# Kernel tuning notes

Hardware: AMD Instinct MI355X
Metric: run time of the kernel (lower is better)

## Reference

```python
import jax, jax.numpy as jnp
import numpy as np


def _chamfer(src, tgt):
    # src: [B, N, 3], tgt: [B, M, 3]
    x2 = jnp.sum(src * src, axis=-1)              # [B, N]
    y2 = jnp.sum(tgt * tgt, axis=-1)              # [B, M]
    xy = jnp.einsum('bnd,bmd->bnm', src, tgt)     # [B, N, M]
    d2 = x2[:, :, None] + y2[:, None, :] - 2.0 * xy
    d2 = jnp.maximum(d2, 0.0)                     # guard tiny negatives
    cham_x = jnp.min(d2, axis=2)                  # [B, N] min over tgt
    cham_y = jnp.min(d2, axis=1)                  # [B, M] min over src
    # point_reduction='mean', batch_reduction='sum'
    loss = jnp.sum(jnp.mean(cham_x, axis=1)) + jnp.sum(jnp.mean(cham_y, axis=1))
    return loss


def setup_inputs() -> dict:
    key = jax.random.key(0)
    k1, k2 = jax.random.split(key)
    src = jax.random.normal(k1, (16, 4096, 3), dtype=jnp.float32)
    tgt = jax.random.normal(k2, (16, 4096, 3), dtype=jnp.float32)
    return {"src": src, "tgt": tgt}


def reference(src, tgt):
    wgeo = 1.0
    return wgeo * _chamfer(src, tgt)
```

## Files before the change

### kernel.cpp

```cpp
#include <hip/hip_runtime.h>
#include <hip/hip_bf16.h>


#define BATCH  16
#define NPTS   4096
#define NPER   (BATCH * NPTS)
#define CHUNKC 512
#define NCHUNKS (NPTS / CHUNKC)

typedef __attribute__((ext_vector_type(8)))  short short8;
typedef __attribute__((ext_vector_type(16))) float float16;

union U4S8 { uint4 u; short8 s; };

__device__ inline unsigned int bfb(float v) {
    __hip_bfloat16 h = __float2bfloat16(v);
    unsigned short u; __builtin_memcpy(&u, &h, 2);
    return (unsigned int)u;
}
__device__ inline float bff(float v) { return __bfloat162float(__float2bfloat16(v)); }

#define ONEB 0x3F80u

__global__ __launch_bounds__(256) void aug_kernel(
    const float* __restrict__ src, const float* __restrict__ tgt,
    uint4* __restrict__ layAlo, uint4* __restrict__ layAhi,
    uint4* __restrict__ layBlo, uint4* __restrict__ layBhi)
{
    int i = blockIdx.x * 256 + threadIdx.x;
    int role = i >> 16;
    int p = i & (NPER - 1);
    const float* base = role ? tgt : src;
    float x = base[3 * p + 0];
    float y = base[3 * p + 1];
    float z = base[3 * p + 2];

    float xhf = bff(x), yhf = bff(y), zhf = bff(z);
    float xlf = x - xhf, ylf = y - yhf, zlf = z - zhf;
    float f = fmaf(x, x, fmaf(y, y, z * z));
    float fhf = bff(f), flf = f - fhf;

    unsigned xh = bfb(xhf), yh = bfb(yhf), zh = bfb(zhf);
    unsigned xl = bfb(xlf), yl = bfb(ylf), zl = bfb(zlf);
    unsigned fh = bfb(fhf), fl = bfb(flf);

    uint4 aw0 = make_uint4(xh | (yh << 16), zh | (xh << 16),
                           yh | (zh << 16), xl | (yl << 16));
    uint4 aw1 = make_uint4(zl | (fh << 16), fl | (ONEB << 16), ONEB, 0u);
    unsigned a = bfb(-2.0f * xhf), b = bfb(-2.0f * yhf), c = bfb(-2.0f * zhf);
    unsigned d = bfb(-2.0f * xlf), e = bfb(-2.0f * ylf), g = bfb(-2.0f * zlf);
    uint4 bw0 = make_uint4(a | (b << 16), c | (d << 16),
                           e | (g << 16), a | (b << 16));
    uint4 bw1 = make_uint4(c | (ONEB << 16), ONEB | (fh << 16), fl, 0u);

    layAlo[i] = aw0; layAhi[i] = aw1;
    layBlo[i] = bw0; layBhi[i] = bw1;
}

__global__ __launch_bounds__(256, 4) void chamfer_mfma_kernel(
    const uint4* __restrict__ layAlo, const uint4* __restrict__ layAhi,
    const uint4* __restrict__ layBlo, const uint4* __restrict__ layBhi,
    float* __restrict__ out)
{
    __shared__ uint4 sbuf[2][2][CHUNKC];
    __shared__ float wsum[4];

    int blk = blockIdx.x;
    const int strip = blk & 31; blk >>= 5;
    const int b     = blk & 15; blk >>= 4;
    const int dir   = blk;

    const int lane = threadIdx.x & 63;
    const int w    = threadIdx.x >> 6;
    const int half = lane >> 5;
    const int l5   = lane & 31;

    const size_t Aoff = (size_t)dir * NPER + (size_t)b * NPTS;
    const size_t Boff = (size_t)(1 - dir) * NPER + (size_t)b * NPTS;

    U4S8 at; at.u = (half ? layAhi : layAlo)[Aoff + strip * 128 + w * 32 + l5];
    const short8 afr = at.s;

    const uint4* Blo = layBlo + Boff;
    const uint4* Bhi = layBhi + Boff;

    auto stage = [&](int c, int bi) {
#pragma unroll
        for (int j = 0; j < 4; j++) {
            int li = w * 256 + j * 64;
            int hf = li >> 9;
            int pt = li & (CHUNKC - 1);
            const uint4* gsrc = (hf ? Bhi : Blo) + c * CHUNKC + pt + lane;
            __builtin_amdgcn_global_load_lds(
                (const __attribute__((address_space(1))) unsigned int*)gsrc,
                (__attribute__((address_space(3))) unsigned int*)&sbuf[bi][hf][pt],
                16, 0, 0);
        }
    };

    const float16 z16 = {0.f,0.f,0.f,0.f,0.f,0.f,0.f,0.f,
                         0.f,0.f,0.f,0.f,0.f,0.f,0.f,0.f};
    float rm[16];
#pragma unroll
    for (int r = 0; r < 16; r++) rm[r] = 1e30f;

    stage(0, 0);
    for (int c = 0; c < NCHUNKS; c++) {
        __syncthreads();
        if (c + 1 < NCHUNKS) stage(c + 1, (c + 1) & 1);
        const int bi = c & 1;
#pragma unroll 2
        for (int j2 = 0; j2 < CHUNKC / 64; j2++) {
            U4S8 t0, t1;
            t0.u = sbuf[bi][half][j2 * 64 + l5];
            t1.u = sbuf[bi][half][j2 * 64 + 32 + l5];
            float16 a0 = __builtin_amdgcn_mfma_f32_32x32x16_bf16(afr, t0.s, z16, 0, 0, 0);
            float16 a1 = __builtin_amdgcn_mfma_f32_32x32x16_bf16(afr, t1.s, z16, 0, 0, 0);
#pragma unroll
            for (int r = 0; r < 16; r++)
                rm[r] = fminf(fminf(a0[r], a1[r]), rm[r]);
        }
    }

#pragma unroll
    for (int mask = 1; mask <= 16; mask <<= 1)
#pragma unroll
        for (int r = 0; r < 16; r++)
            rm[r] = fminf(rm[r], __shfl_xor(rm[r], mask, 64));

    float s = 0.0f;
#pragma unroll
    for (int r = 0; r < 16; r++) s += fmaxf(rm[r], 0.0f);
    s += __shfl_xor(s, 32, 64);

    if (lane == 0) wsum[w] = s;
    __syncthreads();
    if (threadIdx.x == 0)
        atomicAdd(out, (wsum[0] + wsum[1] + wsum[2] + wsum[3]) * (1.0f / (float)NPTS));
}

extern "C" void kernel_launch(void* const* d_in, const int* in_sizes, int n_in,
                              void* d_out, int out_size, void* d_ws, size_t ws_size,
                              hipStream_t stream)
{
    const float* src = (const float*)d_in[0];
    const float* tgt = (const float*)d_in[1];
    float* out = (float*)d_out;

    uint4* layAlo = (uint4*)d_ws;
    uint4* layAhi = layAlo + 2 * NPER;
    uint4* layBlo = layAhi + 2 * NPER;
    uint4* layBhi = layBlo + 2 * NPER;

    hipMemsetAsync(out, 0, sizeof(float), stream);
    aug_kernel<<<2 * NPER / 256, 256, 0, stream>>>(src, tgt,
                                                   layAlo, layAhi, layBlo, layBhi);
    chamfer_mfma_kernel<<<2 * BATCH * 32, 256, 0, stream>>>(layAlo, layAhi,
                                                            layBlo, layBhi, out);
}
```

Before: 88.18 us.

## Fuse bf16 split-layout prep into chamfer MFMA kernel and double rows per wave

Removes the separate augmentation kernel and its workspace round trip. The main kernel now reads raw xyz and builds the bf16 hi/lo augmented operands in registers, for its A rows and for each B chunk as it is written to LDS. Each wave now handles two 32-row A fragments, so every LDS B fragment feeds twice as many MFMAs, and the grid shrinks to 16 strips per batch and direction. The cost is redundant B conversion in every block, plain synchronous stores instead of async global-to-LDS loads, and more registers, with launch bounds lowered to 2 blocks per CU.

```diff
diff --git a/kernel.cpp b/kernel.cpp
--- a/kernel.cpp
+++ b/kernel.cpp
@@ -2,11 +2,11 @@
 #include <hip/hip_bf16.h>
 
 
-#define BATCH  16
-#define NPTS   4096
-#define NPER   (BATCH * NPTS)
-#define CHUNKC 512
+#define BATCH   16
+#define NPTS    4096
+#define CHUNKC  512
 #define NCHUNKS (NPTS / CHUNKC)
+#define NSTRIPS 16
 
 typedef __attribute__((ext_vector_type(8)))  short short8;
 typedef __attribute__((ext_vector_type(16))) float float16;
@@ -22,52 +22,41 @@
 
 #define ONEB 0x3F80u
 
-__global__ __launch_bounds__(256) void aug_kernel(
-    const float* __restrict__ src, const float* __restrict__ tgt,
-    uint4* __restrict__ layAlo, uint4* __restrict__ layAhi,
-    uint4* __restrict__ layBlo, uint4* __restrict__ layBhi)
-{
-    int i = blockIdx.x * 256 + threadIdx.x;
-    int role = i >> 16;
-    int p = i & (NPER - 1);
-    const float* base = role ? tgt : src;
-    float x = base[3 * p + 0];
-    float y = base[3 * p + 1];
-    float z = base[3 * p + 2];
-
+__device__ inline void buildA(float x, float y, float z, uint4& w0, uint4& w1) {
     float xhf = bff(x), yhf = bff(y), zhf = bff(z);
-    float xlf = x - xhf, ylf = y - yhf, zlf = z - zhf;
     float f = fmaf(x, x, fmaf(y, y, z * z));
-    float fhf = bff(f), flf = f - fhf;
-
+    float fhf = bff(f);
     unsigned xh = bfb(xhf), yh = bfb(yhf), zh = bfb(zhf);
-    unsigned xl = bfb(xlf), yl = bfb(ylf), zl = bfb(zlf);
-    unsigned fh = bfb(fhf), fl = bfb(flf);
-
-    uint4 aw0 = make_uint4(xh | (yh << 16), zh | (xh << 16),
-                           yh | (zh << 16), xl | (yl << 16));
-    uint4 aw1 = make_uint4(zl | (fh << 16), fl | (ONEB << 16), ONEB, 0u);
-    unsigned a = bfb(-2.0f * xhf), b = bfb(-2.0f * yhf), c = bfb(-2.0f * zhf);
-    unsigned d = bfb(-2.0f * xlf), e = bfb(-2.0f * ylf), g = bfb(-2.0f * zlf);
-    uint4 bw0 = make_uint4(a | (b << 16), c | (d << 16),
-                           e | (g << 16), a | (b << 16));
-    uint4 bw1 = make_uint4(c | (ONEB << 16), ONEB | (fh << 16), fl, 0u);
-
-    layAlo[i] = aw0; layAhi[i] = aw1;
-    layBlo[i] = bw0; layBhi[i] = bw1;
+    unsigned xl = bfb(x - xhf), yl = bfb(y - yhf), zl = bfb(z - zhf);
+    unsigned fh = bfb(fhf), fl = bfb(f - fhf);
+    w0 = make_uint4(xh | (yh << 16), zh | (xh << 16),
+                    yh | (zh << 16), xl | (yl << 16));
+    w1 = make_uint4(zl | (fh << 16), fl | (ONEB << 16), ONEB, 0u);
 }
 
-__global__ __launch_bounds__(256, 4) void chamfer_mfma_kernel(
-    const uint4* __restrict__ layAlo, const uint4* __restrict__ layAhi,
-    const uint4* __restrict__ layBlo, const uint4* __restrict__ layBhi,
+__device__ inline void buildB(float x, float y, float z, uint4& w0, uint4& w1) {
+    float xhf = bff(x), yhf = bff(y), zhf = bff(z);
+    float f = fmaf(x, x, fmaf(y, y, z * z));
+    float fhf = bff(f);
+    unsigned a = bfb(-2.0f * xhf), b = bfb(-2.0f * yhf), c = bfb(-2.0f * zhf);
+    unsigned d = bfb(-2.0f * (x - xhf)), e = bfb(-2.0f * (y - yhf)),
+             g = bfb(-2.0f * (z - zhf));
+    unsigned fh = bfb(fhf), fl = bfb(f - fhf);
+    w0 = make_uint4(a | (b << 16), c | (d << 16),
+                    e | (g << 16), a | (b << 16));
+    w1 = make_uint4(c | (ONEB << 16), ONEB | (fh << 16), fl, 0u);
+}
+
+__global__ __launch_bounds__(256, 2) void chamfer_fused_kernel(
+    const float* __restrict__ src, const float* __restrict__ tgt,
     float* __restrict__ out)
 {
     __shared__ uint4 sbuf[2][2][CHUNKC];
     __shared__ float wsum[4];
 
     int blk = blockIdx.x;
-    const int strip = blk & 31; blk >>= 5;
-    const int b     = blk & 15; blk >>= 4;
+    const int strip = blk & (NSTRIPS - 1); blk >>= 4;
+    const int b     = blk & 15;            blk >>= 4;
     const int dir   = blk;
 
     const int lane = threadIdx.x & 63;
@@ -75,62 +64,74 @@
     const int half = lane >> 5;
     const int l5   = lane & 31;
 
-    const size_t Aoff = (size_t)dir * NPER + (size_t)b * NPTS;
-    const size_t Boff = (size_t)(1 - dir) * NPER + (size_t)b * NPTS;
+    const float* Araw = (dir ? tgt : src) + (size_t)b * NPTS * 3;
+    const float* Braw = (dir ? src : tgt) + (size_t)b * NPTS * 3;
 
-    U4S8 at; at.u = (half ? layAhi : layAlo)[Aoff + strip * 128 + w * 32 + l5];
-    const short8 afr = at.s;
+    short8 afr[2];
+#pragma unroll
+    for (int g = 0; g < 2; g++) {
+        int row = strip * 256 + g * 128 + w * 32 + l5;
+        uint4 w0, w1;
+        buildA(Araw[3 * row], Araw[3 * row + 1], Araw[3 * row + 2], w0, w1);
+        U4S8 t; t.u = half ? w1 : w0;
+        afr[g] = t.s;
+    }
 
-    const uint4* Blo = layBlo + Boff;
-    const uint4* Bhi = layBhi + Boff;
-
-    auto stage = [&](int c, int bi) {
+    auto convert = [&](int c, int bi) {
 #pragma unroll
-        for (int j = 0; j < 4; j++) {
-            int li = w * 256 + j * 64;
-            int hf = li >> 9;
-            int pt = li & (CHUNKC - 1);
-            const uint4* gsrc = (hf ? Bhi : Blo) + c * CHUNKC + pt + lane;
-            __builtin_amdgcn_global_load_lds(
-                (const __attribute__((address_space(1))) unsigned int*)gsrc,
-                (__attribute__((address_space(3))) unsigned int*)&sbuf[bi][hf][pt],
-                16, 0, 0);
+        for (int k = 0; k < 2; k++) {
+            int lp = (int)threadIdx.x + k * 256;
+            int p  = c * CHUNKC + lp;
+            uint4 w0, w1;
+            buildB(Braw[3 * p], Braw[3 * p + 1], Braw[3 * p + 2], w0, w1);
+            sbuf[bi][0][lp] = w0;
+            sbuf[bi][1][lp] = w1;
         }
     };
 
     const float16 z16 = {0.f,0.f,0.f,0.f,0.f,0.f,0.f,0.f,
                          0.f,0.f,0.f,0.f,0.f,0.f,0.f,0.f};
-    float rm[16];
+    float rm[2][16];
 #pragma unroll
-    for (int r = 0; r < 16; r++) rm[r] = 1e30f;
+    for (int g = 0; g < 2; g++)
+#pragma unroll
+        for (int r = 0; r < 16; r++) rm[g][r] = 1e30f;
 
-    stage(0, 0);
+    convert(0, 0);
     for (int c = 0; c < NCHUNKS; c++) {
         __syncthreads();
-        if (c + 1 < NCHUNKS) stage(c + 1, (c + 1) & 1);
+        if (c + 1 < NCHUNKS) convert(c + 1, (c + 1) & 1);
         const int bi = c & 1;
 #pragma unroll 2
         for (int j2 = 0; j2 < CHUNKC / 64; j2++) {
             U4S8 t0, t1;
             t0.u = sbuf[bi][half][j2 * 64 + l5];
             t1.u = sbuf[bi][half][j2 * 64 + 32 + l5];
-            float16 a0 = __builtin_amdgcn_mfma_f32_32x32x16_bf16(afr, t0.s, z16, 0, 0, 0);
-            float16 a1 = __builtin_amdgcn_mfma_f32_32x32x16_bf16(afr, t1.s, z16, 0, 0, 0);
+            float16 a00 = __builtin_amdgcn_mfma_f32_32x32x16_bf16(afr[0], t0.s, z16, 0, 0, 0);
+            float16 a01 = __builtin_amdgcn_mfma_f32_32x32x16_bf16(afr[0], t1.s, z16, 0, 0, 0);
+            float16 a10 = __builtin_amdgcn_mfma_f32_32x32x16_bf16(afr[1], t0.s, z16, 0, 0, 0);
+            float16 a11 = __builtin_amdgcn_mfma_f32_32x32x16_bf16(afr[1], t1.s, z16, 0, 0, 0);
 #pragma unroll
-            for (int r = 0; r < 16; r++)
-                rm[r] = fminf(fminf(a0[r], a1[r]), rm[r]);
+            for (int r = 0; r < 16; r++) {
+                rm[0][r] = fminf(fminf(a00[r], a01[r]), rm[0][r]);
+                rm[1][r] = fminf(fminf(a10[r], a11[r]), rm[1][r]);
+            }
         }
     }
 
 #pragma unroll
     for (int mask = 1; mask <= 16; mask <<= 1)
 #pragma unroll
-        for (int r = 0; r < 16; r++)
-            rm[r] = fminf(rm[r], __shfl_xor(rm[r], mask, 64));
+        for (int g = 0; g < 2; g++)
+#pragma unroll
+            for (int r = 0; r < 16; r++)
+                rm[g][r] = fminf(rm[g][r], __shfl_xor(rm[g][r], mask, 64));
 
     float s = 0.0f;
 #pragma unroll
-    for (int r = 0; r < 16; r++) s += fmaxf(rm[r], 0.0f);
+    for (int g = 0; g < 2; g++)
+#pragma unroll
+        for (int r = 0; r < 16; r++) s += fmaxf(rm[g][r], 0.0f);
     s += __shfl_xor(s, 32, 64);
 
     if (lane == 0) wsum[w] = s;
@@ -147,14 +148,6 @@
     const float* tgt = (const float*)d_in[1];
     float* out = (float*)d_out;
 
-    uint4* layAlo = (uint4*)d_ws;
-    uint4* layAhi = layAlo + 2 * NPER;
-    uint4* layBlo = layAhi + 2 * NPER;
-    uint4* layBhi = layBlo + 2 * NPER;
-
     hipMemsetAsync(out, 0, sizeof(float), stream);
-    aug_kernel<<<2 * NPER / 256, 256, 0, stream>>>(src, tgt,
-                                                   layAlo, layAhi, layBlo, layBhi);
-    chamfer_mfma_kernel<<<2 * BATCH * 32, 256, 0, stream>>>(layAlo, layAhi,
-                                                            layBlo, layBhi, out);
+    chamfer_fused_kernel<<<2 * BATCH * NSTRIPS, 256, 0, stream>>>(src, tgt, out);
 }
```

Measured after the change: 79.71 us. 9.6% less time.
